# Kernel tuning notes

Hardware: AMD Instinct MI355X
Metric: run time of the kernel (lower is better)

Reference implementation:

```python
import jax, jax.numpy as jnp
import numpy as np

N_QUBITS = 12
N_LAYERS = 6
BATCH = 256
INPUT_DIM = 256
OUT_DIM = 64
PI = float(np.pi)


def _ry_mat(a):
    # a: scalar or (B,) real angle -> (...,2,2) complex64 RY matrix
    c, s = jnp.cos(a * 0.5), jnp.sin(a * 0.5)
    return jnp.stack([jnp.stack([c, -s], -1), jnp.stack([s, c], -1)], -2).astype(jnp.complex64)


def _rz_mat(a):
    # diag(e^{-i a/2}, e^{+i a/2})
    em = jnp.exp(-0.5j * a.astype(jnp.complex64))
    ep = jnp.exp(0.5j * a.astype(jnp.complex64))
    z = jnp.zeros_like(em)
    return jnp.stack([jnp.stack([em, z], -1), jnp.stack([z, ep], -1)], -2)


def _apply_1q(state, U, w):
    # shared (2,2) gate on wire w; state: (B, 2, ..., 2)
    s = jnp.moveaxis(state, w + 1, -1)
    s = jnp.einsum('ij,b...j->b...i', U, s)
    return jnp.moveaxis(s, -1, w + 1)


def _apply_1q_batched(state, U, w):
    # per-sample (B,2,2) gate on wire w
    s = jnp.moveaxis(state, w + 1, -1)
    s = jnp.einsum('bij,b...j->b...i', U, s)
    return jnp.moveaxis(s, -1, w + 1)


def _cnot(state, c, t):
    s0 = jnp.take(state, 0, axis=c + 1)
    s1 = jnp.take(state, 1, axis=c + 1)
    t_ax = t + 1 if t < c else t  # target axis index after removing control axis
    s1 = jnp.flip(s1, axis=t_ax)
    return jnp.stack([s0, s1], axis=c + 1)


def _cz(state, c, t):
    idx = [slice(None)] * (N_QUBITS + 1)
    idx[c + 1] = 1
    idx[t + 1] = 1
    return state.at[tuple(idx)].multiply(-1.0)


def _run_circuit(xq, q_weights):
    # xq: (B, n_qubits) in [-1,1]; forward passes xq*pi, circuit multiplies by pi again
    B = xq.shape[0]
    enc = xq * (PI * PI)
    state = jnp.zeros((B, 2 ** N_QUBITS), jnp.complex64).at[:, 0].set(1.0)
    state = state.reshape((B,) + (2,) * N_QUBITS)
    for i in range(N_QUBITS):
        state = _apply_1q_batched(state, _ry_mat(enc[:, i]), i)
    w = q_weights.reshape(N_LAYERS, N_QUBITS, 3)
    for layer in range(N_LAYERS):
        for i in range(N_QUBITS):
            # PennyLane order: RZ(w0) then RY(w1) then RZ(w2) -> U = RZ2 @ RY1 @ RZ0
            U = _rz_mat(w[layer, i, 2]) @ _ry_mat(w[layer, i, 1]) @ _rz_mat(w[layer, i, 0])
            state = _apply_1q(state, U, i)
        for i in range(N_QUBITS):
            state = _cnot(state, i, (i + 1) % N_QUBITS)
        if layer % 2 == 0 and layer < N_LAYERS - 1:
            for i in range(N_QUBITS):
                state = _apply_1q_batched(state, _ry_mat(enc[:, i] * 0.5), i)
        if layer % 2 == 1:
            for i in range(0, N_QUBITS - 2, 2):
                state = _cz(state, i, i + 2)
    # PauliZ expectation on wires 0,1,2
    p = (state.real ** 2 + state.imag ** 2).reshape(B, 2, 2, 2, -1).sum(-1)  # (B,2,2,2)
    z0 = (p[:, 0] - p[:, 1]).sum((-1, -2))
    z1 = (p[:, :, 0] - p[:, :, 1]).sum((-1, -2))
    z2 = (p[:, :, :, 0] - p[:, :, :, 1]).sum((-1, -2))
    return jnp.stack([z0, z1, z2], -1)  # (B, 3) float32


def _layernorm(h, g, b, eps=1e-5):
    mu = h.mean(-1, keepdims=True)
    var = ((h - mu) ** 2).mean(-1, keepdims=True)
    return (h - mu) * jax.lax.rsqrt(var + eps) * g + b


def _forward(x, W1, b1, g_ln, b_ln, W2, b2, W3, b3, q_weights, W4, b4, W5, b5):
    gelu = lambda t: jax.nn.gelu(t, approximate=False)
    h = gelu(x @ W1.T + b1)
    h = _layernorm(h, g_ln, b_ln)
    h = gelu(h @ W2.T + b2)
    xq = jnp.tanh(h @ W3.T + b3)  # (B, n_qubits)
    q = _run_circuit(xq, q_weights)  # (B, 3)
    return gelu(q @ W4.T + b4) @ W5.T + b5  # (B, OUT_DIM)


def setup_inputs() -> dict:
    key = jax.random.key(0)
    ks = jax.random.split(key, 8)
    rn = lambda k, shape, s=0.05: (jax.random.normal(k, shape) * s).astype(jnp.float32)
    return {
        'x': jax.random.normal(ks[0], (BATCH, INPUT_DIM), jnp.float32),
        'W1': rn(ks[1], (128, INPUT_DIM)), 'b1': jnp.zeros(128, jnp.float32),
        'g_ln': jnp.ones(128, jnp.float32), 'b_ln': jnp.zeros(128, jnp.float32),
        'W2': rn(ks[2], (64, 128)), 'b2': jnp.zeros(64, jnp.float32),
        'W3': rn(ks[3], (N_QUBITS, 64)), 'b3': jnp.zeros(N_QUBITS, jnp.float32),
        'q_weights': (jax.random.normal(ks[4], (N_LAYERS * N_QUBITS * 3,)) * 0.1).astype(jnp.float32),
        'W4': rn(ks[5], (32, 3)), 'b4': jnp.zeros(32, jnp.float32),
        'W5': rn(ks[6], (OUT_DIM, 32)), 'b5': jnp.zeros(OUT_DIM, jnp.float32),
    }


def reference(x, W1, b1, g_ln, b_ln, W2, b2, W3, b3, q_weights, W4, b4, W5, b5):
    return _forward(x, W1, b1, g_ln, b_ln, W2, b2, W3, b3, q_weights, W4, b4, W5, b5)
```

## Files before the change

### kernel.cpp

```cpp
#include <hip/hip_runtime.h>
#include <math.h>

#define NQ   12
#define NL   6
#define DIM  4096
#define BATCH 256
#define NT   512
#define PI2  9.869604401089358f

__device__ __forceinline__ float geluf(float x) {
    return 0.5f * x * (1.0f + erff(x * 0.70710678118654752f));
}

__device__ __forceinline__ float2 cmul(float2 a, float2 b) {
    return make_float2(fmaf(a.x, b.x, -a.y * b.y), fmaf(a.x, b.y, a.y * b.x));
}
__device__ __forceinline__ float2 cadd(float2 a, float2 b) {
    return make_float2(a.x + b.x, a.y + b.y);
}
__device__ __forceinline__ float2 cscale(float2 a, float s) {
    return make_float2(a.x * s, a.y * s);
}

__device__ __forceinline__ int gmap(int j) {
    return ((j ^ (j >> 1)) & 0x3FF)
         | ((((j >> 10) ^ (j >> 11) ^ j) & 1) << 10)
         | ((((j >> 11) ^ j) & 1) << 11);
}

template<int CTRL>
__device__ __forceinline__ float2 dppx(float2 v) {
    int x = __builtin_amdgcn_update_dpp(0, __float_as_int(v.x), CTRL, 0xF, 0xF, true);
    int y = __builtin_amdgcn_update_dpp(0, __float_as_int(v.y), CTRL, 0xF, 0xF, true);
    return make_float2(__int_as_float(x), __int_as_float(y));
}

__device__ __forceinline__ float2 shflx(float2 v, int mask) {
    return make_float2(__shfl_xor(v.x, mask, 64), __shfl_xor(v.y, mask, 64));
}

__device__ __forceinline__ void reg_gate(float2* a, const float2* Ug, int bit) {
    const float2 u00 = Ug[0], u01 = Ug[1], u10 = Ug[2], u11 = Ug[3];
    #pragma unroll
    for (int m = 0; m < 8; m++) {
        if (m & bit) continue;
        float2 x0 = a[m], x1 = a[m | bit];
        a[m]       = cadd(cmul(u00, x0), cmul(u01, x1));
        a[m | bit] = cadd(cmul(u10, x0), cmul(u11, x1));
    }
}

__global__ __launch_bounds__(NT)
void qpu_kernel(const float* __restrict__ x,   const float* __restrict__ W1, const float* __restrict__ b1,
                const float* __restrict__ g_ln, const float* __restrict__ b_ln,
                const float* __restrict__ W2,  const float* __restrict__ b2,
                const float* __restrict__ W3,  const float* __restrict__ b3,
                const float* __restrict__ qw,  const float* __restrict__ W4, const float* __restrict__ b4,
                const float* __restrict__ W5,  const float* __restrict__ b5,
                float* __restrict__ out)
{
    __shared__ float2 bufA[4352];
    __shared__ float2 bufB[4352];
    __shared__ float2 Um[NL * NQ * 4];
    __shared__ float  xs[256];
    __shared__ float  h1n[128];
    __shared__ float  h2s[64];
    __shared__ float  xqs[NQ];
    __shared__ float  musd[2];
    __shared__ float  qv[3];
    __shared__ float  h4s[32];
    __shared__ float  zred[8][3];

    const int t = threadIdx.x;
    const int b = blockIdx.x;

    if (t < 256) xs[t] = x[b * 256 + t];
    __syncthreads();

    if (t < 128) {
        const float4* w = (const float4*)(W1 + t * 256);
        float a0 = 0.f, a1 = 0.f, a2 = 0.f, a3 = 0.f;
        #pragma unroll 8
        for (int k = 0; k < 64; k++) {
            float4 wv = w[k];
            const float* xp = &xs[4 * k];
            a0 = fmaf(wv.x, xp[0], a0);
            a1 = fmaf(wv.y, xp[1], a1);
            a2 = fmaf(wv.z, xp[2], a2);
            a3 = fmaf(wv.w, xp[3], a3);
        }
        h1n[t] = geluf((a0 + a1) + (a2 + a3) + b1[t]);
    }
    __syncthreads();

    if (t < 64) {
        float v0 = h1n[t], v1 = h1n[t + 64];
        float s1 = v0 + v1;
        float s2 = fmaf(v0, v0, v1 * v1);
        #pragma unroll
        for (int off = 32; off > 0; off >>= 1) {
            s1 += __shfl_down(s1, off);
            s2 += __shfl_down(s2, off);
        }
        if (t == 0) {
            float mu  = s1 * (1.f / 128.f);
            float var = s2 * (1.f / 128.f) - mu * mu;
            musd[0] = mu;
            musd[1] = rsqrtf(var + 1e-5f);
        }
    }
    __syncthreads();
    if (t < 128) h1n[t] = (h1n[t] - musd[0]) * musd[1] * g_ln[t] + b_ln[t];
    __syncthreads();

    if (t < 64) {
        const float4* w = (const float4*)(W2 + t * 128);
        float a0 = 0.f, a1 = 0.f, a2 = 0.f, a3 = 0.f;
        #pragma unroll 8
        for (int k = 0; k < 32; k++) {
            float4 wv = w[k];
            const float* hp = &h1n[4 * k];
            a0 = fmaf(wv.x, hp[0], a0);
            a1 = fmaf(wv.y, hp[1], a1);
            a2 = fmaf(wv.z, hp[2], a2);
            a3 = fmaf(wv.w, hp[3], a3);
        }
        h2s[t] = geluf((a0 + a1) + (a2 + a3) + b2[t]);
    }
    __syncthreads();

    if (t < NQ) {
        const float4* w = (const float4*)(W3 + t * 64);
        float a0 = 0.f, a1 = 0.f, a2 = 0.f, a3 = 0.f;
        #pragma unroll
        for (int k = 0; k < 16; k++) {
            float4 wv = w[k];
            const float* hp = &h2s[4 * k];
            a0 = fmaf(wv.x, hp[0], a0);
            a1 = fmaf(wv.y, hp[1], a1);
            a2 = fmaf(wv.z, hp[2], a2);
            a3 = fmaf(wv.w, hp[3], a3);
        }
        xqs[t] = tanhf((a0 + a1) + (a2 + a3) + b3[t]);
    }
    __syncthreads();

    if (t < NL * NQ) {
        const int l = t / NQ;
        const int i = t % NQ;
        float a  = qw[t * 3 + 0];
        float bb = qw[t * 3 + 1];
        float c  = qw[t * 3 + 2];
        float sb, cb;   sincosf(0.5f * bb, &sb, &cb);
        float apc = 0.5f * (a + c), amc = 0.5f * (a - c);
        float sapc, capc; sincosf(apc, &sapc, &capc);
        float samc, camc; sincosf(amc, &samc, &camc);
        float2 u00 = make_float2( cb * capc, -cb * sapc);
        float2 u01 = make_float2(-sb * camc, -sb * samc);
        float2 u10 = make_float2( sb * camc, -sb * samc);
        float2 u11 = make_float2( cb * capc,  cb * sapc);

        float theta = 0.f;
        bool merge = false;
        if (l == 0)      { theta = xqs[i] * PI2;        merge = true; }
        else if (l & 1)  { theta = xqs[i] * PI2 * 0.5f; merge = true; }
        if (merge) {
            float sy, cy; sincosf(0.5f * theta, &sy, &cy);
            float2 m00 = cadd(cscale(u00,  cy), cscale(u01, sy));
            float2 m01 = cadd(cscale(u00, -sy), cscale(u01, cy));
            float2 m10 = cadd(cscale(u10,  cy), cscale(u11, sy));
            float2 m11 = cadd(cscale(u10, -sy), cscale(u11, cy));
            u00 = m00; u01 = m01; u10 = m10; u11 = m11;
        }
        Um[t * 4 + 0] = u00;
        Um[t * 4 + 1] = u01;
        Um[t * 4 + 2] = u10;
        Um[t * 4 + 3] = u11;
    }
    __syncthreads();

    float2 a[8];
    {
        const float2* U0 = Um;
        float2 P = ((t >> 0) & 1) ? U0[11 * 4 + 2] : U0[11 * 4 + 0];
        #pragma unroll
        for (int bb = 1; bb < 9; bb++) {
            const float2* Uq = &U0[(11 - bb) * 4];
            float2 fac = ((t >> bb) & 1) ? Uq[2] : Uq[0];
            P = cmul(P, fac);
        }
        float2 b0 = cmul(P, U0[2 * 4 + 0]);
        float2 b1 = cmul(P, U0[2 * 4 + 2]);
        float2 a00 = cmul(b0, U0[1 * 4 + 0]);
        float2 a01 = cmul(b1, U0[1 * 4 + 0]);
        float2 a10 = cmul(b0, U0[1 * 4 + 2]);
        float2 a11 = cmul(b1, U0[1 * 4 + 2]);
        float2 f11 = U0[0 * 4 + 0], g11 = U0[0 * 4 + 2];
        a[0] = cmul(a00, f11); a[1] = cmul(a01, f11);
        a[2] = cmul(a10, f11); a[3] = cmul(a11, f11);
        a[4] = cmul(a00, g11); a[5] = cmul(a01, g11);
        a[6] = cmul(a10, g11); a[7] = cmul(a11, g11);
    }

    {
        float2* wa = &bufA[t + (t >> 4)];
        #pragma unroll
        for (int m = 0; m < 8; m++) wa[m * 544] = a[m];
        __syncthreads();
        #pragma unroll
        for (int m = 0; m < 8; m++) {
            const int src = gmap(8 * t + m);
            a[m] = bufA[src + (src >> 4)];
        }
    }

    #pragma unroll 1
    for (int l = 1; l < NL; l++) {
        const float2* UL = &Um[l * NQ * 4];

        reg_gate(a, &UL[11 * 4], 1);
        reg_gate(a, &UL[10 * 4], 2);
        reg_gate(a, &UL[ 9 * 4], 4);

        #pragma unroll
        for (int k = 0; k < 6; k++) {
            const float2* Ug = &UL[(8 - k) * 4];
            const float2 u00 = Ug[0], u01 = Ug[1], u10 = Ug[2], u11 = Ug[3];
            const bool sel = (t >> k) & 1;
            const float2 cA = sel ? u11 : u00;
            const float2 cB = sel ? u10 : u01;
            #pragma unroll
            for (int m = 0; m < 8; m++) {
                float2 v;
                if      (k == 0) v = dppx<0xB1>(a[m]);
                else if (k == 1) v = dppx<0x4E>(a[m]);
                else             v = shflx(a[m], 1 << k);
                a[m] = cadd(cmul(cA, a[m]), cmul(cB, v));
            }
        }

        {
            float2* wb = &bufB[8 * t + (t >> 1)];
            #pragma unroll
            for (int m = 0; m < 8; m++) wb[m] = a[m];
            __syncthreads();
            const float2* rb = &bufB[t + (t >> 4)];
            #pragma unroll
            for (int m = 0; m < 8; m++) a[m] = rb[m * 544];
        }

        reg_gate(a, &UL[2 * 4], 1);
        reg_gate(a, &UL[1 * 4], 2);
        reg_gate(a, &UL[0 * 4], 4);

        if (l < NL - 1) {
            float2* wa = &bufA[t + (t >> 4)];
            #pragma unroll
            for (int m = 0; m < 8; m++) wa[m * 544] = a[m];
            __syncthreads();
            const bool czl = (l == 1) || (l == 3);
            #pragma unroll
            for (int m = 0; m < 8; m++) {
                const int j = 8 * t + m;
                const int src = gmap(j);
                float2 v = bufA[src + (src >> 4)];
                if (czl && (__popc(j & (j << 2) & 0xAA8) & 1)) { v.x = -v.x; v.y = -v.y; }
                a[m] = v;
            }
        }
    }

    float p[8];
    #pragma unroll
    for (int m = 0; m < 8; m++) p[m] = fmaf(a[m].x, a[m].x, a[m].y * a[m].y);

    float s03 = (p[0] - p[1] - p[2] + p[3]) + (p[4] - p[5] - p[6] + p[7]);
    float z0 = (__popc(t) & 1) ? -s03 : s03;
    float z1 = (p[0] + p[1]) - (p[2] + p[3]) - (p[4] + p[5]) + (p[6] + p[7]);
    float z2 = (p[0] - p[1] - p[2] + p[3]) - (p[4] - p[5] - p[6] + p[7]);

    #pragma unroll
    for (int off = 32; off > 0; off >>= 1) {
        z0 += __shfl_down(z0, off);
        z1 += __shfl_down(z1, off);
        z2 += __shfl_down(z2, off);
    }
    if ((t & 63) == 0) {
        zred[t >> 6][0] = z0;
        zred[t >> 6][1] = z1;
        zred[t >> 6][2] = z2;
    }
    __syncthreads();
    if (t == 0) {
        float q0 = 0.f, q1 = 0.f, q2 = 0.f;
        #pragma unroll
        for (int w = 0; w < 8; w++) {
            q0 += zred[w][0]; q1 += zred[w][1]; q2 += zred[w][2];
        }
        qv[0] = q0; qv[1] = q1; qv[2] = q2;
    }
    __syncthreads();

    if (t < 32) {
        float h = b4[t];
        h = fmaf(qv[0], W4[t * 3 + 0], h);
        h = fmaf(qv[1], W4[t * 3 + 1], h);
        h = fmaf(qv[2], W4[t * 3 + 2], h);
        h4s[t] = geluf(h);
    }
    __syncthreads();
    if (t < 64) {
        float acc = b5[t];
        #pragma unroll
        for (int h = 0; h < 32; h++) acc = fmaf(h4s[h], W5[t * 32 + h], acc);
        out[b * 64 + t] = acc;
    }
}

extern "C" void kernel_launch(void* const* d_in, const int* in_sizes, int n_in,
                              void* d_out, int out_size, void* d_ws, size_t ws_size,
                              hipStream_t stream) {
    (void)in_sizes; (void)n_in; (void)d_ws; (void)ws_size; (void)out_size;
    const float* x    = (const float*)d_in[0];
    const float* W1   = (const float*)d_in[1];
    const float* b1   = (const float*)d_in[2];
    const float* g_ln = (const float*)d_in[3];
    const float* b_ln = (const float*)d_in[4];
    const float* W2   = (const float*)d_in[5];
    const float* b2   = (const float*)d_in[6];
    const float* W3   = (const float*)d_in[7];
    const float* b3   = (const float*)d_in[8];
    const float* qw   = (const float*)d_in[9];
    const float* W4   = (const float*)d_in[10];
    const float* b4   = (const float*)d_in[11];
    const float* W5   = (const float*)d_in[12];
    const float* b5   = (const float*)d_in[13];
    float* out = (float*)d_out;

    qpu_kernel<<<BATCH, NT, 0, stream>>>(x, W1, b1, g_ln, b_ln, W2, b2,
                                         W3, b3, qw, W4, b4, W5, b5, out);
}
```

Measured before the change: 110.3 us.

## Double threads to 1024 with 4 amplitudes per thread and split MLP dot products

Raises the block to 1024 threads so each thread holds 4 statevector amplitudes instead of 8. Cross-lane gates now use DPP, ds_swizzle and a single xor-32 shuffle, with a new sigma permutation and padded shared-memory transposes. The MLP layers split each dot product across 8 threads with a shared partial-sum reduction, and the initial product state is computed directly per amplitude. This is meant to cut per-thread serial work and latency in the single-block-per-sample kernel, at the cost of more register pressure limits per block, extra barriers, and lower occupancy per CU.

```diff
diff --git a/kernel.cpp b/kernel.cpp
--- a/kernel.cpp
+++ b/kernel.cpp
@@ -3,29 +3,34 @@
 
 #define NQ   12
 #define NL   6
-#define DIM  4096
 #define BATCH 256
-#define NT   512
+#define NT   1024
 #define PI2  9.869604401089358f
 
 __device__ __forceinline__ float geluf(float x) {
     return 0.5f * x * (1.0f + erff(x * 0.70710678118654752f));
 }
 
-__device__ __forceinline__ float2 cmul(float2 a, float2 b) {
-    return make_float2(fmaf(a.x, b.x, -a.y * b.y), fmaf(a.x, b.y, a.y * b.x));
-}
-__device__ __forceinline__ float2 cadd(float2 a, float2 b) {
-    return make_float2(a.x + b.x, a.y + b.y);
-}
-__device__ __forceinline__ float2 cscale(float2 a, float s) {
-    return make_float2(a.x * s, a.y * s);
+__device__ __forceinline__ int Pad(int x) { return x + (x >> 4) + (x >> 8); }
+
+__device__ __forceinline__ int sigma(int x) {
+    return (x & 0xC3) | ((x & 0x3C) << 6) | ((x >> 6) & 0x3C);
 }
 
 __device__ __forceinline__ int gmap(int j) {
     return ((j ^ (j >> 1)) & 0x3FF)
          | ((((j >> 10) ^ (j >> 11) ^ j) & 1) << 10)
          | ((((j >> 11) ^ j) & 1) << 11);
+}
+
+__device__ __forceinline__ float2 cmul(float2 a, float2 b) {
+    return make_float2(fmaf(a.x, b.x, -a.y * b.y), fmaf(a.x, b.y, a.y * b.x));
+}
+__device__ __forceinline__ float2 cadd(float2 a, float2 b) {
+    return make_float2(a.x + b.x, a.y + b.y);
+}
+__device__ __forceinline__ float2 cscale(float2 a, float s) {
+    return make_float2(a.x * s, a.y * s);
 }
 
 template<int CTRL>
@@ -34,19 +39,53 @@
     int y = __builtin_amdgcn_update_dpp(0, __float_as_int(v.y), CTRL, 0xF, 0xF, true);
     return make_float2(__int_as_float(x), __int_as_float(y));
 }
-
-__device__ __forceinline__ float2 shflx(float2 v, int mask) {
-    return make_float2(__shfl_xor(v.x, mask, 64), __shfl_xor(v.y, mask, 64));
-}
-
-__device__ __forceinline__ void reg_gate(float2* a, const float2* Ug, int bit) {
+template<int OFF>
+__device__ __forceinline__ float2 swzx(float2 v) {
+    int x = __builtin_amdgcn_ds_swizzle(__float_as_int(v.x), OFF);
+    int y = __builtin_amdgcn_ds_swizzle(__float_as_int(v.y), OFF);
+    return make_float2(__int_as_float(x), __int_as_float(y));
+}
+__device__ __forceinline__ float2 shflx32(float2 v) {
+    return make_float2(__shfl_xor(v.x, 32, 64), __shfl_xor(v.y, 32, 64));
+}
+
+__device__ __forceinline__ void gate_reg(float2* a, const float2* Ug, int bit) {
     const float2 u00 = Ug[0], u01 = Ug[1], u10 = Ug[2], u11 = Ug[3];
     #pragma unroll
-    for (int m = 0; m < 8; m++) {
+    for (int m = 0; m < 4; m++) {
         if (m & bit) continue;
         float2 x0 = a[m], x1 = a[m | bit];
         a[m]       = cadd(cmul(u00, x0), cmul(u01, x1));
         a[m | bit] = cadd(cmul(u10, x0), cmul(u11, x1));
+    }
+}
+template<int CTRL>
+__device__ __forceinline__ void gate_dpp(float2* a, const float2* Ug, bool sel) {
+    const float2 cA = sel ? Ug[3] : Ug[0];
+    const float2 cB = sel ? Ug[2] : Ug[1];
+    #pragma unroll
+    for (int m = 0; m < 4; m++) {
+        float2 v = dppx<CTRL>(a[m]);
+        a[m] = cadd(cmul(cA, a[m]), cmul(cB, v));
+    }
+}
+template<int OFF>
+__device__ __forceinline__ void gate_swz(float2* a, const float2* Ug, bool sel) {
+    const float2 cA = sel ? Ug[3] : Ug[0];
+    const float2 cB = sel ? Ug[2] : Ug[1];
+    #pragma unroll
+    for (int m = 0; m < 4; m++) {
+        float2 v = swzx<OFF>(a[m]);
+        a[m] = cadd(cmul(cA, a[m]), cmul(cB, v));
+    }
+}
+__device__ __forceinline__ void gate_shfl32(float2* a, const float2* Ug, bool sel) {
+    const float2 cA = sel ? Ug[3] : Ug[0];
+    const float2 cB = sel ? Ug[2] : Ug[1];
+    #pragma unroll
+    for (int m = 0; m < 4; m++) {
+        float2 v = shflx32(a[m]);
+        a[m] = cadd(cmul(cA, a[m]), cmul(cB, v));
     }
 }
 
@@ -59,17 +98,18 @@
                 const float* __restrict__ W5,  const float* __restrict__ b5,
                 float* __restrict__ out)
 {
-    __shared__ float2 bufA[4352];
-    __shared__ float2 bufB[4352];
+    __shared__ float2 bufA[4368];
+    __shared__ float2 bufB[4368];
     __shared__ float2 Um[NL * NQ * 4];
     __shared__ float  xs[256];
+    __shared__ float  pr[128 * 9];
     __shared__ float  h1n[128];
     __shared__ float  h2s[64];
     __shared__ float  xqs[NQ];
     __shared__ float  musd[2];
     __shared__ float  qv[3];
     __shared__ float  h4s[32];
-    __shared__ float  zred[8][3];
+    __shared__ float  zred[16][3];
 
     const int t = threadIdx.x;
     const int b = blockIdx.x;
@@ -77,19 +117,27 @@
     if (t < 256) xs[t] = x[b * 256 + t];
     __syncthreads();
 
+    {
+        const int o = t >> 3, part = t & 7;
+        const float4* w = (const float4*)(W1 + o * 256) + part * 8;
+        const float*  xp = xs + part * 32;
+        float a0 = 0.f, a1 = 0.f, a2 = 0.f, a3 = 0.f;
+        #pragma unroll
+        for (int k = 0; k < 8; k++) {
+            float4 wv = w[k];
+            a0 = fmaf(wv.x, xp[4 * k + 0], a0);
+            a1 = fmaf(wv.y, xp[4 * k + 1], a1);
+            a2 = fmaf(wv.z, xp[4 * k + 2], a2);
+            a3 = fmaf(wv.w, xp[4 * k + 3], a3);
+        }
+        pr[o * 9 + part] = (a0 + a1) + (a2 + a3);
+    }
+    __syncthreads();
     if (t < 128) {
-        const float4* w = (const float4*)(W1 + t * 256);
-        float a0 = 0.f, a1 = 0.f, a2 = 0.f, a3 = 0.f;
-        #pragma unroll 8
-        for (int k = 0; k < 64; k++) {
-            float4 wv = w[k];
-            const float* xp = &xs[4 * k];
-            a0 = fmaf(wv.x, xp[0], a0);
-            a1 = fmaf(wv.y, xp[1], a1);
-            a2 = fmaf(wv.z, xp[2], a2);
-            a3 = fmaf(wv.w, xp[3], a3);
-        }
-        h1n[t] = geluf((a0 + a1) + (a2 + a3) + b1[t]);
+        float s = 0.f;
+        #pragma unroll
+        for (int k = 0; k < 8; k++) s += pr[t * 9 + k];
+        h1n[t] = geluf(s + b1[t]);
     }
     __syncthreads();
 
@@ -113,35 +161,48 @@
     if (t < 128) h1n[t] = (h1n[t] - musd[0]) * musd[1] * g_ln[t] + b_ln[t];
     __syncthreads();
 
+    if (t < 512) {
+        const int o = t >> 3, part = t & 7;
+        const float4* w = (const float4*)(W2 + o * 128) + part * 4;
+        const float*  hp = h1n + part * 16;
+        float a0 = 0.f, a1 = 0.f, a2 = 0.f, a3 = 0.f;
+        #pragma unroll
+        for (int k = 0; k < 4; k++) {
+            float4 wv = w[k];
+            a0 = fmaf(wv.x, hp[4 * k + 0], a0);
+            a1 = fmaf(wv.y, hp[4 * k + 1], a1);
+            a2 = fmaf(wv.z, hp[4 * k + 2], a2);
+            a3 = fmaf(wv.w, hp[4 * k + 3], a3);
+        }
+        pr[o * 9 + part] = (a0 + a1) + (a2 + a3);
+    }
+    __syncthreads();
     if (t < 64) {
-        const float4* w = (const float4*)(W2 + t * 128);
-        float a0 = 0.f, a1 = 0.f, a2 = 0.f, a3 = 0.f;
-        #pragma unroll 8
-        for (int k = 0; k < 32; k++) {
-            float4 wv = w[k];
-            const float* hp = &h1n[4 * k];
-            a0 = fmaf(wv.x, hp[0], a0);
-            a1 = fmaf(wv.y, hp[1], a1);
-            a2 = fmaf(wv.z, hp[2], a2);
-            a3 = fmaf(wv.w, hp[3], a3);
-        }
-        h2s[t] = geluf((a0 + a1) + (a2 + a3) + b2[t]);
-    }
-    __syncthreads();
-
+        float s = 0.f;
+        #pragma unroll
+        for (int k = 0; k < 8; k++) s += pr[t * 9 + k];
+        h2s[t] = geluf(s + b2[t]);
+    }
+    __syncthreads();
+
+    if (t < 96) {
+        const int o = t >> 3, part = t & 7;
+        const float4* w = (const float4*)(W3 + o * 64) + part * 2;
+        const float*  hp = h2s + part * 8;
+        float4 w0 = w[0], w1 = w[1];
+        float s = 0.f;
+        s = fmaf(w0.x, hp[0], s); s = fmaf(w0.y, hp[1], s);
+        s = fmaf(w0.z, hp[2], s); s = fmaf(w0.w, hp[3], s);
+        s = fmaf(w1.x, hp[4], s); s = fmaf(w1.y, hp[5], s);
+        s = fmaf(w1.z, hp[6], s); s = fmaf(w1.w, hp[7], s);
+        pr[o * 9 + part] = s;
+    }
+    __syncthreads();
     if (t < NQ) {
-        const float4* w = (const float4*)(W3 + t * 64);
-        float a0 = 0.f, a1 = 0.f, a2 = 0.f, a3 = 0.f;
-        #pragma unroll
-        for (int k = 0; k < 16; k++) {
-            float4 wv = w[k];
-            const float* hp = &h2s[4 * k];
-            a0 = fmaf(wv.x, hp[0], a0);
-            a1 = fmaf(wv.y, hp[1], a1);
-            a2 = fmaf(wv.z, hp[2], a2);
-            a3 = fmaf(wv.w, hp[3], a3);
-        }
-        xqs[t] = tanhf((a0 + a1) + (a2 + a3) + b3[t]);
+        float s = 0.f;
+        #pragma unroll
+        for (int k = 0; k < 8; k++) s += pr[t * 9 + k];
+        xqs[t] = tanhf(s + b3[t]);
     }
     __syncthreads();
 
@@ -179,106 +240,73 @@
     }
     __syncthreads();
 
-    float2 a[8];
-    {
-        const float2* U0 = Um;
-        float2 P = ((t >> 0) & 1) ? U0[11 * 4 + 2] : U0[11 * 4 + 0];
-        #pragma unroll
-        for (int bb = 1; bb < 9; bb++) {
-            const float2* Uq = &U0[(11 - bb) * 4];
-            float2 fac = ((t >> bb) & 1) ? Uq[2] : Uq[0];
-            P = cmul(P, fac);
-        }
-        float2 b0 = cmul(P, U0[2 * 4 + 0]);
-        float2 b1 = cmul(P, U0[2 * 4 + 2]);
-        float2 a00 = cmul(b0, U0[1 * 4 + 0]);
-        float2 a01 = cmul(b1, U0[1 * 4 + 0]);
-        float2 a10 = cmul(b0, U0[1 * 4 + 2]);
-        float2 a11 = cmul(b1, U0[1 * 4 + 2]);
-        float2 f11 = U0[0 * 4 + 0], g11 = U0[0 * 4 + 2];
-        a[0] = cmul(a00, f11); a[1] = cmul(a01, f11);
-        a[2] = cmul(a10, f11); a[3] = cmul(a11, f11);
-        a[4] = cmul(a00, g11); a[5] = cmul(a01, g11);
-        a[6] = cmul(a10, g11); a[7] = cmul(a11, g11);
-    }
-
-    {
-        float2* wa = &bufA[t + (t >> 4)];
-        #pragma unroll
-        for (int m = 0; m < 8; m++) wa[m * 544] = a[m];
-        __syncthreads();
-        #pragma unroll
-        for (int m = 0; m < 8; m++) {
-            const int src = gmap(8 * t + m);
-            a[m] = bufA[src + (src >> 4)];
-        }
+    float2 a[4];
+    #pragma unroll
+    for (int m = 0; m < 4; m++) {
+        const int i = gmap(4 * t + m);
+        float2 acc = (i & 1) ? Um[11 * 4 + 2] : Um[11 * 4 + 0];
+        #pragma unroll
+        for (int bb = 1; bb < 12; bb++) {
+            const float2* Uq = &Um[(11 - bb) * 4];
+            float2 f = ((i >> bb) & 1) ? Uq[2] : Uq[0];
+            acc = cmul(acc, f);
+        }
+        a[m] = acc;
     }
 
     #pragma unroll 1
     for (int l = 1; l < NL; l++) {
         const float2* UL = &Um[l * NQ * 4];
 
-        reg_gate(a, &UL[11 * 4], 1);
-        reg_gate(a, &UL[10 * 4], 2);
-        reg_gate(a, &UL[ 9 * 4], 4);
-
-        #pragma unroll
-        for (int k = 0; k < 6; k++) {
-            const float2* Ug = &UL[(8 - k) * 4];
-            const float2 u00 = Ug[0], u01 = Ug[1], u10 = Ug[2], u11 = Ug[3];
-            const bool sel = (t >> k) & 1;
-            const float2 cA = sel ? u11 : u00;
-            const float2 cB = sel ? u10 : u01;
+        gate_reg(a, &UL[11 * 4], 1);
+        gate_reg(a, &UL[10 * 4], 2);
+        gate_dpp<0xB1>  (a, &UL[9 * 4], (t >> 0) & 1);
+        gate_dpp<0x4E>  (a, &UL[8 * 4], (t >> 1) & 1);
+        gate_swz<0x101F>(a, &UL[7 * 4], (t >> 2) & 1);
+        gate_dpp<0x128> (a, &UL[6 * 4], (t >> 3) & 1);
+        gate_swz<0x401F>(a, &UL[5 * 4], (t >> 4) & 1);
+        gate_shfl32     (a, &UL[4 * 4], (t >> 5) & 1);
+
+        {
+            const int base = Pad(4 * t);
             #pragma unroll
-            for (int m = 0; m < 8; m++) {
-                float2 v;
-                if      (k == 0) v = dppx<0xB1>(a[m]);
-                else if (k == 1) v = dppx<0x4E>(a[m]);
-                else             v = shflx(a[m], 1 << k);
-                a[m] = cadd(cmul(cA, a[m]), cmul(cB, v));
-            }
-        }
-
-        {
-            float2* wb = &bufB[8 * t + (t >> 1)];
+            for (int m = 0; m < 4; m++) bufB[base + m] = a[m];
+            __syncthreads();
+            const int sb = Pad(sigma(4 * t));
             #pragma unroll
-            for (int m = 0; m < 8; m++) wb[m] = a[m];
-            __syncthreads();
-            const float2* rb = &bufB[t + (t >> 4)];
+            for (int m = 0; m < 4; m++) a[m] = bufB[sb + m];
+        }
+
+        gate_dpp<0xB1>  (a, &UL[3 * 4], (t >> 0) & 1);
+        gate_dpp<0x4E>  (a, &UL[2 * 4], (t >> 1) & 1);
+        gate_swz<0x101F>(a, &UL[1 * 4], (t >> 2) & 1);
+        gate_dpp<0x128> (a, &UL[0 * 4], (t >> 3) & 1);
+
+        if (l < NL - 1) {
+            const int sb = Pad(sigma(4 * t));
             #pragma unroll
-            for (int m = 0; m < 8; m++) a[m] = rb[m * 544];
-        }
-
-        reg_gate(a, &UL[2 * 4], 1);
-        reg_gate(a, &UL[1 * 4], 2);
-        reg_gate(a, &UL[0 * 4], 4);
-
-        if (l < NL - 1) {
-            float2* wa = &bufA[t + (t >> 4)];
-            #pragma unroll
-            for (int m = 0; m < 8; m++) wa[m * 544] = a[m];
+            for (int m = 0; m < 4; m++) bufA[sb + m] = a[m];
             __syncthreads();
             const bool czl = (l == 1) || (l == 3);
             #pragma unroll
-            for (int m = 0; m < 8; m++) {
-                const int j = 8 * t + m;
-                const int src = gmap(j);
-                float2 v = bufA[src + (src >> 4)];
+            for (int m = 0; m < 4; m++) {
+                const int j = 4 * t + m;
+                float2 v = bufA[Pad(gmap(j))];
                 if (czl && (__popc(j & (j << 2) & 0xAA8) & 1)) { v.x = -v.x; v.y = -v.y; }
                 a[m] = v;
             }
         }
     }
 
-    float p[8];
-    #pragma unroll
-    for (int m = 0; m < 8; m++) p[m] = fmaf(a[m].x, a[m].x, a[m].y * a[m].y);
-
-    float s03 = (p[0] - p[1] - p[2] + p[3]) + (p[4] - p[5] - p[6] + p[7]);
-    float z0 = (__popc(t) & 1) ? -s03 : s03;
-    float z1 = (p[0] + p[1]) - (p[2] + p[3]) - (p[4] + p[5]) + (p[6] + p[7]);
-    float z2 = (p[0] - p[1] - p[2] + p[3]) - (p[4] - p[5] - p[6] + p[7]);
-
+    float z0 = 0.f, z1 = 0.f, z2 = 0.f;
+    #pragma unroll
+    for (int m = 0; m < 4; m++) {
+        const int j = sigma(4 * t + m);
+        float p = fmaf(a[m].x, a[m].x, a[m].y * a[m].y);
+        z0 += (__popc(j & 0x7FF) & 1) ? -p : p;
+        z1 += (__popc(j & 0xC00) & 1) ? -p : p;
+        z2 += (__popc(j & 0xE00) & 1) ? -p : p;
+    }
     #pragma unroll
     for (int off = 32; off > 0; off >>= 1) {
         z0 += __shfl_down(z0, off);
@@ -294,7 +322,7 @@
     if (t == 0) {
         float q0 = 0.f, q1 = 0.f, q2 = 0.f;
         #pragma unroll
-        for (int w = 0; w < 8; w++) {
+        for (int w = 0; w < 16; w++) {
             q0 += zred[w][0]; q1 += zred[w][1]; q2 += zred[w][2];
         }
         qv[0] = q0; qv[1] = q1; qv[2] = q2;
```

Measured after the change: 105.8 us. 1.04x faster.
